# Performance work log

Measured on AMD Instinct MI355X. Metric: run time of the kernel, lower is better.

The kernel has to match this reference:

```python
import jax, jax.numpy as jnp
import numpy as np

HEADS = 8
REL_MAX = 64  # module-level constant REL_MAX_DIST


def _to_c(x):
    # x: [..., 2] real/imag interleaved (torch.view_as_real layout) -> complex
    return jax.lax.complex(x[..., 0], x[..., 1])


def setup_inputs() -> dict:
    key = jax.random.key(0)
    ks = jax.random.split(key, 12)
    dim, past_len = 256, 65536
    d2 = dim * 2
    s = 1.0 / np.sqrt(d2)  # torch Linear default init range

    def lin(k):
        kw, kb = jax.random.split(k)
        W = jax.random.uniform(kw, (d2, d2), jnp.float32, -s, s)
        b = jax.random.uniform(kb, (d2,), jnp.float32, -s, s)
        return W, b

    Wq, bq = lin(ks[0])
    Wk, bk = lin(ks[1])
    Wv, bv = lin(ks[2])
    Wo, bo = lin(ks[3])
    return {
        "curr_pos": past_len,
        "z_curr": jax.random.normal(ks[4], (dim, 2), jnp.float32),
        "z_past": jax.random.normal(ks[5], (past_len, dim, 2), jnp.float32),
        "Wq": Wq, "bq": bq, "Wk": Wk, "bk": bk,
        "Wv": Wv, "bv": bv, "Wo": Wo, "bo": bo,
        "rel_bias": jax.random.normal(ks[6], (2 * REL_MAX + 1, dim, 2), jnp.float32) * 0.02,
    }


def reference(curr_pos, z_curr, z_past, Wq, bq, Wk, bk, Wv, bv, Wo, bo, rel_bias):
    dim = z_curr.shape[0]
    past_len = z_past.shape[0]
    head_dim = dim // HEADS

    # real-valued linear projections on interleaved (real, imag) features
    q_proj = z_curr.reshape(-1) @ Wq.T + bq                        # [2*dim]
    k_proj = z_past.reshape(past_len, -1) @ Wk.T + bk              # [L, 2*dim]
    v_proj = z_past.reshape(past_len, -1) @ Wv.T + bv              # [L, 2*dim]

    # view as complex, split heads
    q_h = _to_c(q_proj.reshape(dim, 2)).reshape(HEADS, head_dim)               # [H, hd]
    k_h = _to_c(k_proj.reshape(past_len, dim, 2)).reshape(past_len, HEADS, head_dim)
    v_h = _to_c(v_proj.reshape(past_len, dim, 2)).reshape(past_len, HEADS, head_dim)

    # Re(<q, k>) per head
    dot_scores = jnp.real(jnp.conj(q_h)[None] * k_h).sum(-1)       # [L, H]

    # relative positional bias (gather + clamp)
    rel_dists = jnp.arange(curr_pos - past_len, curr_pos)
    idx = jnp.clip(rel_dists + REL_MAX, 0, 2 * REL_MAX)
    rb_h = _to_c(rel_bias)[idx].reshape(past_len, HEADS, head_dim)
    rel_scores = jnp.real(jnp.conj(q_h)[None] * rb_h).sum(-1)      # [L, H]

    scores = (dot_scores + rel_scores) / np.sqrt(head_dim)
    weights = jax.nn.softmax(scores, axis=0)                       # softmax over past_len

    out_h = (weights[..., None] * v_h).sum(0)                      # [H, hd] complex
    out_c = out_h.reshape(dim)
    out_real = jnp.stack([jnp.real(out_c), jnp.imag(out_c)], -1).reshape(-1)  # [2*dim]
    out = out_real @ Wo.T + bo
    # return real view [dim, 2] of the complex output (view_as_complex layout)
    return out.reshape(dim, 2)
```

## Files before the change

### kernel.cpp

```cpp
#include <hip/hip_runtime.h>
#include <math.h>


static constexpr float SCALE = 0.17677669529663687f;

__device__ __forceinline__ float wave_sum(float v) {
#pragma unroll
  for (int off = 32; off > 0; off >>= 1) v += __shfl_xor(v, off, 64);
  return v;
}

__global__ __launch_bounds__(256) void k_matvec512(
    const float* __restrict__ M, const float* __restrict__ x,
    const float* __restrict__ bias, float* __restrict__ y) {
  const int wave = threadIdx.x >> 6, lane = threadIdx.x & 63;
  const int j = blockIdx.x * 4 + wave;
  const float* Mr = M + (size_t)j * 512 + lane * 8;
  const float4 m0 = *(const float4*)Mr;
  const float4 m1 = *(const float4*)(Mr + 4);
  const float4 x0 = *(const float4*)(x + lane * 8);
  const float4 x1 = *(const float4*)(x + lane * 8 + 4);
  float acc = m0.x * x0.x + m0.y * x0.y + m0.z * x0.z + m0.w * x0.w +
              m1.x * x1.x + m1.y * x1.y + m1.z * x1.z + m1.w * x1.w;
  acc = wave_sum(acc);
  if (lane == 0) y[j] = acc + bias[j];
}

__global__ __launch_bounds__(256) void k_wkpart(
    const float* __restrict__ Wk, const float* __restrict__ qp,
    float* __restrict__ wkpart) {
  __shared__ float ql[32];
  const int b = blockIdx.x;
  if (threadIdx.x < 32) ql[threadIdx.x] = qp[b * 32 + threadIdx.x];
  __syncthreads();
  for (int i = threadIdx.x; i < 512; i += 256) {
    float acc = 0.f;
#pragma unroll
    for (int k = 0; k < 32; ++k)
      acc += ql[k] * Wk[(size_t)(b * 32 + k) * 512 + i];
    wkpart[b * 512 + i] = acc;
  }
}

__global__ __launch_bounds__(256) void k_misc(
    const float* __restrict__ qp, const float* __restrict__ bk,
    const float* __restrict__ rb, const float* __restrict__ wkpart,
    float* __restrict__ wk, float* __restrict__ ck, float* __restrict__ relq,
    float* __restrict__ S_un) {
  const int b = blockIdx.x;
  if (b < 8) {
    for (int i = threadIdx.x; i < 512; i += 256)
      wk[b * 512 + i] =
          (wkpart[(2 * b) * 512 + i] + wkpart[(2 * b + 1) * 512 + i]) * SCALE;
  } else if (b == 8) {
    if (threadIdx.x < 8) {
      const int h = threadIdx.x;
      float acc = 0.f;
      for (int k = 0; k < 64; ++k) acc += qp[h * 64 + k] * bk[h * 64 + k];
      ck[h] = acc * SCALE;
    }
  } else if (b < 14) {
    const int t = (b - 9) * 256 + threadIdx.x;
    if (t < 129 * 8) {
      const int idx = t >> 3, h = t & 7;
      float acc = 0.f;
      for (int k = 0; k < 64; ++k)
        acc += qp[h * 64 + k] * rb[(size_t)idx * 512 + h * 64 + k];
      relq[t] = acc * SCALE;
    }
  } else {
    for (int t = threadIdx.x; t < 4096; t += 256) S_un[t] = 0.f;
  }
}

__global__ __launch_bounds__(256, 2) void k_attn(
    const float* __restrict__ zp, const float* __restrict__ wk,
    const float* __restrict__ ck, const float* __restrict__ relq,
    const int* __restrict__ curr_pos, int L, float* __restrict__ Sp,
    float* __restrict__ sp) {
  __shared__ float relql[1032];
  __shared__ float Sl[4096];
  __shared__ float sl[4][8];
  const int tid = threadIdx.x;
  const int wave = tid >> 6, lane = tid & 63;
  for (int t = tid; t < 1032; t += 256) relql[t] = relq[t];

  float wkr[8][8];
#pragma unroll
  for (int h = 0; h < 8; ++h) {
    const float4 a = *(const float4*)(wk + h * 512 + lane * 8);
    const float4 b = *(const float4*)(wk + h * 512 + lane * 8 + 4);
    wkr[h][0] = a.x; wkr[h][1] = a.y; wkr[h][2] = a.z; wkr[h][3] = a.w;
    wkr[h][4] = b.x; wkr[h][5] = b.y; wkr[h][6] = b.z; wkr[h][7] = b.w;
  }
  const int myh = ((lane & 1) << 2) | (lane & 2) | ((lane >> 2) & 1);
  const float ck_my = ck[myh];
  const int cp = curr_pos[0];
  __syncthreads();

  float S[8][8];
#pragma unroll
  for (int h = 0; h < 8; ++h)
#pragma unroll
    for (int k = 0; k < 8; ++k) S[h][k] = 0.f;
  float s_loc = 0.f;

  const int l0 = blockIdx.x * 128 + wave * 32;
  const float* zr = zp + (size_t)l0 * 512 + lane * 8;
  float4 p0 = *(const float4*)zr;
  float4 p1 = *(const float4*)(zr + 4);

#pragma unroll 2
  for (int r = 0; r < 32; ++r) {
    const int l = l0 + r;
    const float* zn = (l + 1 < L) ? (zr + 512) : zr;
    const float4 n0 = *(const float4*)zn;
    const float4 n1 = *(const float4*)(zn + 4);
    const float zz[8] = {p0.x, p0.y, p0.z, p0.w, p1.x, p1.y, p1.z, p1.w};
    float acc[8];
#pragma unroll
    for (int h = 0; h < 8; ++h) {
      float a = 0.f;
#pragma unroll
      for (int k = 0; k < 8; ++k) a += zz[k] * wkr[h][k];
      acc[h] = a;
    }
    const bool lo1 = (lane & 1) == 0;
    float b0 = (lo1 ? acc[0] : acc[4]) + __shfl_xor(lo1 ? acc[4] : acc[0], 1, 64);
    float b1 = (lo1 ? acc[1] : acc[5]) + __shfl_xor(lo1 ? acc[5] : acc[1], 1, 64);
    float b2 = (lo1 ? acc[2] : acc[6]) + __shfl_xor(lo1 ? acc[6] : acc[2], 1, 64);
    float b3 = (lo1 ? acc[3] : acc[7]) + __shfl_xor(lo1 ? acc[7] : acc[3], 1, 64);
    const bool lo2 = (lane & 2) == 0;
    float c0 = (lo2 ? b0 : b2) + __shfl_xor(lo2 ? b2 : b0, 2, 64);
    float c1 = (lo2 ? b1 : b3) + __shfl_xor(lo2 ? b3 : b1, 2, 64);
    const bool lo3 = (lane & 4) == 0;
    float d = (lo3 ? c0 : c1) + __shfl_xor(lo3 ? c1 : c0, 4, 64);
    d += __shfl_xor(d, 8, 64);
    d += __shfl_xor(d, 16, 64);
    d += __shfl_xor(d, 32, 64);

    int dd = cp - L + l + 64;
    dd = dd < 0 ? 0 : (dd > 128 ? 128 : dd);
    float w = __expf(d + ck_my + relql[dd * 8 + myh]);
    if (l >= L) w = 0.f;
    s_loc += w;
#pragma unroll
    for (int h = 0; h < 8; ++h) {
      const int src = ((h & 1) << 2) | (h & 2) | ((h >> 2) & 1);
      const float wh = __shfl(w, src, 64);
#pragma unroll
      for (int k = 0; k < 8; ++k) S[h][k] += wh * zz[k];
    }
    p0 = n0; p1 = n1; zr += 512;
  }

  if (lane < 8) sl[wave][myh] = s_loc;
  for (int wv = 0; wv < 4; ++wv) {
    if (wave == wv) {
#pragma unroll
      for (int h = 0; h < 8; ++h)
#pragma unroll
        for (int k = 0; k < 8; ++k) {
          const int idx = h * 512 + lane * 8 + k;
          if (wv == 0) Sl[idx] = S[h][k];
          else Sl[idx] += S[h][k];
        }
    }
    __syncthreads();
  }
  for (int t = tid; t < 4096; t += 256)
    Sp[(size_t)blockIdx.x * 4096 + t] = Sl[t];
  if (tid < 8)
    sp[blockIdx.x * 8 + tid] = sl[0][tid] + sl[1][tid] + sl[2][tid] + sl[3][tid];
}

__global__ __launch_bounds__(256) void k_comb2(
    const float* __restrict__ Sp, const float* __restrict__ spv, int nb,
    float* __restrict__ S_un, float* __restrict__ s) {
  if (blockIdx.x < 256) {
    const int T = blockIdx.x * 256 + threadIdx.x;
    const int col = T & 4095;
    const int g = T >> 12;
    const int chunk = (nb + 15) >> 4;
    const int r0 = g * chunk;
    const int r1 = min(r0 + chunk, nb);
    float a[8];
#pragma unroll
    for (int u = 0; u < 8; ++u) a[u] = 0.f;
    int b = r0;
    for (; b + 8 <= r1; b += 8) {
#pragma unroll
      for (int u = 0; u < 8; ++u) a[u] += Sp[(size_t)(b + u) * 4096 + col];
    }
    for (; b < r1; ++b) a[0] += Sp[(size_t)b * 4096 + col];
    const float t = ((a[0] + a[1]) + (a[2] + a[3])) +
                    ((a[4] + a[5]) + (a[6] + a[7]));
    atomicAdd(&S_un[col], t);
  } else {
    __shared__ float red[256];
    float a = 0.f;
    for (int b2 = threadIdx.x >> 3; b2 < nb; b2 += 32)
      a += spv[b2 * 8 + (threadIdx.x & 7)];
    red[threadIdx.x] = a;
    __syncthreads();
    if (threadIdx.x < 8) {
      float x = 0.f;
      for (int c = 0; c < 32; ++c) x += red[c * 8 + threadIdx.x];
      s[threadIdx.x] = x;
    }
  }
}

__global__ __launch_bounds__(256) void k_outreal(
    const float* __restrict__ Wv, const float* __restrict__ S_un,
    const float* __restrict__ s, const float* __restrict__ bv,
    float* __restrict__ out_real) {
  const int wave = threadIdx.x >> 6, lane = threadIdx.x & 63;
  const int j = blockIdx.x * 4 + wave;
  const int h = j >> 6;
  const float* Mr = Wv + (size_t)j * 512 + lane * 8;
  const float* xr = S_un + h * 512 + lane * 8;
  const float4 m0 = *(const float4*)Mr;
  const float4 m1 = *(const float4*)(Mr + 4);
  const float4 x0 = *(const float4*)xr;
  const float4 x1 = *(const float4*)(xr + 4);
  float acc = m0.x * x0.x + m0.y * x0.y + m0.z * x0.z + m0.w * x0.w +
              m1.x * x1.x + m1.y * x1.y + m1.z * x1.z + m1.w * x1.w;
  acc = wave_sum(acc);
  if (lane == 0) out_real[j] = acc / s[h] + bv[j];
}

extern "C" void kernel_launch(void* const* d_in, const int* in_sizes, int n_in,
                              void* d_out, int out_size, void* d_ws,
                              size_t ws_size, hipStream_t stream) {
  const int* curr_pos = (const int*)d_in[0];
  const float* z_curr = (const float*)d_in[1];
  const float* z_past = (const float*)d_in[2];
  const float* Wq = (const float*)d_in[3];
  const float* bq = (const float*)d_in[4];
  const float* Wk = (const float*)d_in[5];
  const float* bk = (const float*)d_in[6];
  const float* Wv = (const float*)d_in[7];
  const float* bv = (const float*)d_in[8];
  const float* Wo = (const float*)d_in[9];
  const float* bo = (const float*)d_in[10];
  const float* rb = (const float*)d_in[11];
  float* out = (float*)d_out;

  const int L = in_sizes[2] / 512;
  const int nb = (L + 127) / 128;

  float* ws = (float*)d_ws;
  size_t o = 0;
  float* qp = ws + o;       o += 512;
  float* wkpart = ws + o;   o += 16 * 512;
  float* wk = ws + o;       o += 8 * 512;
  float* ck = ws + o;       o += 16;
  float* relq = ws + o;     o += 1040;
  float* s = ws + o;        o += 8;
  float* sp = ws + o;       o += (size_t)nb * 8;
  float* S_un = ws + o;     o += 4096;
  float* out_real = ws + o; o += 512;
  float* Sp = ws + o;       o += (size_t)nb * 4096;
  (void)ws_size; (void)n_in; (void)out_size;

  k_matvec512<<<128, 256, 0, stream>>>(Wq, z_curr, bq, qp);
  k_wkpart<<<16, 256, 0, stream>>>(Wk, qp, wkpart);
  k_misc<<<15, 256, 0, stream>>>(qp, bk, rb, wkpart, wk, ck, relq, S_un);
  k_attn<<<nb, 256, 0, stream>>>(z_past, wk, ck, relq, curr_pos, L, Sp, sp);
  k_comb2<<<257, 256, 0, stream>>>(Sp, sp, nb, S_un, s);
  k_outreal<<<128, 256, 0, stream>>>(Wv, S_un, s, bv, out_real);
  k_matvec512<<<128, 256, 0, stream>>>(Wo, out_real, bo, out);
}
```

Baseline: 243.4 us.

## Fuse front kernels, atomically reduce attention partials, prefetch two rows ahead

The change merges the Wk-projection partial and misc setup kernels into one launch, with each block reducing a full head so the separate partial-sum pass goes away. The attention kernel now adds its per-block sums straight into the global accumulator with atomics, which removes the Sp scratch write and the k_comb2 reduction kernel. The z_past prefetch is also deepened to two rows ahead. The cost is heavy atomic contention, since 512 blocks each add into the same 4096 floats, plus nondeterministic summation order and extra registers for the deeper prefetch.

```diff
diff --git a/kernel.cpp b/kernel.cpp
--- a/kernel.cpp
+++ b/kernel.cpp
@@ -26,58 +26,53 @@
   if (lane == 0) y[j] = acc + bias[j];
 }
 
-__global__ __launch_bounds__(256) void k_wkpart(
+__global__ __launch_bounds__(256) void k_front2(
     const float* __restrict__ Wk, const float* __restrict__ qp,
-    float* __restrict__ wkpart) {
-  __shared__ float ql[32];
+    const float* __restrict__ bk, const float* __restrict__ rb,
+    float* __restrict__ wk, float* __restrict__ ck, float* __restrict__ relq,
+    float* __restrict__ S_un, float* __restrict__ s) {
+  __shared__ float ql[512];
   const int b = blockIdx.x;
-  if (threadIdx.x < 32) ql[threadIdx.x] = qp[b * 32 + threadIdx.x];
-  __syncthreads();
-  for (int i = threadIdx.x; i < 512; i += 256) {
+  if (b < 16) {
+    const int h = b >> 1;
+    if (threadIdx.x < 64) ql[threadIdx.x] = qp[h * 64 + threadIdx.x];
+    __syncthreads();
+    const int i = (b & 1) * 256 + threadIdx.x;
     float acc = 0.f;
 #pragma unroll
-    for (int k = 0; k < 32; ++k)
-      acc += ql[k] * Wk[(size_t)(b * 32 + k) * 512 + i];
-    wkpart[b * 512 + i] = acc;
-  }
-}
-
-__global__ __launch_bounds__(256) void k_misc(
-    const float* __restrict__ qp, const float* __restrict__ bk,
-    const float* __restrict__ rb, const float* __restrict__ wkpart,
-    float* __restrict__ wk, float* __restrict__ ck, float* __restrict__ relq,
-    float* __restrict__ S_un) {
-  const int b = blockIdx.x;
-  if (b < 8) {
-    for (int i = threadIdx.x; i < 512; i += 256)
-      wk[b * 512 + i] =
-          (wkpart[(2 * b) * 512 + i] + wkpart[(2 * b + 1) * 512 + i]) * SCALE;
-  } else if (b == 8) {
+    for (int k = 0; k < 64; ++k)
+      acc += ql[k] * Wk[(size_t)(h * 64 + k) * 512 + i];
+    wk[h * 512 + i] = acc * SCALE;
+  } else if (b < 22) {
+    for (int t = threadIdx.x; t < 512; t += 256) ql[t] = qp[t];
+    __syncthreads();
+    const int t = (b - 16) * 256 + threadIdx.x;
+    if (t < 129 * 8) {
+      const int idx = t >> 3, h = t & 7;
+      float acc = 0.f;
+#pragma unroll
+      for (int k = 0; k < 64; ++k)
+        acc += ql[h * 64 + k] * rb[(size_t)idx * 512 + h * 64 + k];
+      relq[t] = acc * SCALE;
+    }
+  } else if (b == 22) {
     if (threadIdx.x < 8) {
       const int h = threadIdx.x;
       float acc = 0.f;
       for (int k = 0; k < 64; ++k) acc += qp[h * 64 + k] * bk[h * 64 + k];
       ck[h] = acc * SCALE;
     }
-  } else if (b < 14) {
-    const int t = (b - 9) * 256 + threadIdx.x;
-    if (t < 129 * 8) {
-      const int idx = t >> 3, h = t & 7;
-      float acc = 0.f;
-      for (int k = 0; k < 64; ++k)
-        acc += qp[h * 64 + k] * rb[(size_t)idx * 512 + h * 64 + k];
-      relq[t] = acc * SCALE;
-    }
   } else {
     for (int t = threadIdx.x; t < 4096; t += 256) S_un[t] = 0.f;
+    if (threadIdx.x < 8) s[threadIdx.x] = 0.f;
   }
 }
 
 __global__ __launch_bounds__(256, 2) void k_attn(
     const float* __restrict__ zp, const float* __restrict__ wk,
     const float* __restrict__ ck, const float* __restrict__ relq,
-    const int* __restrict__ curr_pos, int L, float* __restrict__ Sp,
-    float* __restrict__ sp) {
+    const int* __restrict__ curr_pos, int L, float* __restrict__ S_un,
+    float* __restrict__ s_out) {
   __shared__ float relql[1032];
   __shared__ float Sl[4096];
   __shared__ float sl[4][8];
@@ -109,11 +104,14 @@
   const float* zr = zp + (size_t)l0 * 512 + lane * 8;
   float4 p0 = *(const float4*)zr;
   float4 p1 = *(const float4*)(zr + 4);
+  const float* z1p = (l0 + 1 < L) ? (zr + 512) : zr;
+  float4 q0 = *(const float4*)z1p;
+  float4 q1 = *(const float4*)(z1p + 4);
 
 #pragma unroll 2
   for (int r = 0; r < 32; ++r) {
     const int l = l0 + r;
-    const float* zn = (l + 1 < L) ? (zr + 512) : zr;
+    const float* zn = (l + 2 < L) ? (zr + 1024) : zr;
     const float4 n0 = *(const float4*)zn;
     const float4 n1 = *(const float4*)(zn + 4);
     const float zz[8] = {p0.x, p0.y, p0.z, p0.w, p1.x, p1.y, p1.z, p1.w};
@@ -151,7 +149,7 @@
 #pragma unroll
       for (int k = 0; k < 8; ++k) S[h][k] += wh * zz[k];
     }
-    p0 = n0; p1 = n1; zr += 512;
+    p0 = q0; p1 = q1; q0 = n0; q1 = n1; zr += 512;
   }
 
   if (lane < 8) sl[wave][myh] = s_loc;
@@ -168,47 +166,9 @@
     }
     __syncthreads();
   }
-  for (int t = tid; t < 4096; t += 256)
-    Sp[(size_t)blockIdx.x * 4096 + t] = Sl[t];
+  for (int t = tid; t < 4096; t += 256) atomicAdd(&S_un[t], Sl[t]);
   if (tid < 8)
-    sp[blockIdx.x * 8 + tid] = sl[0][tid] + sl[1][tid] + sl[2][tid] + sl[3][tid];
-}
-
-__global__ __launch_bounds__(256) void k_comb2(
-    const float* __restrict__ Sp, const float* __restrict__ spv, int nb,
-    float* __restrict__ S_un, float* __restrict__ s) {
-  if (blockIdx.x < 256) {
-    const int T = blockIdx.x * 256 + threadIdx.x;
-    const int col = T & 4095;
-    const int g = T >> 12;
-    const int chunk = (nb + 15) >> 4;
-    const int r0 = g * chunk;
-    const int r1 = min(r0 + chunk, nb);
-    float a[8];
-#pragma unroll
-    for (int u = 0; u < 8; ++u) a[u] = 0.f;
-    int b = r0;
-    for (; b + 8 <= r1; b += 8) {
-#pragma unroll
-      for (int u = 0; u < 8; ++u) a[u] += Sp[(size_t)(b + u) * 4096 + col];
-    }
-    for (; b < r1; ++b) a[0] += Sp[(size_t)b * 4096 + col];
-    const float t = ((a[0] + a[1]) + (a[2] + a[3])) +
-                    ((a[4] + a[5]) + (a[6] + a[7]));
-    atomicAdd(&S_un[col], t);
-  } else {
-    __shared__ float red[256];
-    float a = 0.f;
-    for (int b2 = threadIdx.x >> 3; b2 < nb; b2 += 32)
-      a += spv[b2 * 8 + (threadIdx.x & 7)];
-    red[threadIdx.x] = a;
-    __syncthreads();
-    if (threadIdx.x < 8) {
-      float x = 0.f;
-      for (int c = 0; c < 32; ++c) x += red[c * 8 + threadIdx.x];
-      s[threadIdx.x] = x;
-    }
-  }
+    atomicAdd(&s_out[tid], sl[0][tid] + sl[1][tid] + sl[2][tid] + sl[3][tid]);
 }
 
 __global__ __launch_bounds__(256) void k_outreal(
@@ -253,22 +213,17 @@
   float* ws = (float*)d_ws;
   size_t o = 0;
   float* qp = ws + o;       o += 512;
-  float* wkpart = ws + o;   o += 16 * 512;
-  float* wk = ws + o;       o += 8 * 512;
-  float* ck = ws + o;       o += 16;
+  float* wkb = ws + o;      o += 8 * 512;
+  float* ckb = ws + o;      o += 16;
   float* relq = ws + o;     o += 1040;
-  float* s = ws + o;        o += 8;
-  float* sp = ws + o;       o += (size_t)nb * 8;
+  float* sb = ws + o;       o += 8;
   float* S_un = ws + o;     o += 4096;
   float* out_real = ws + o; o += 512;
-  float* Sp = ws + o;       o += (size_t)nb * 4096;
   (void)ws_size; (void)n_in; (void)out_size;
 
   k_matvec512<<<128, 256, 0, stream>>>(Wq, z_curr, bq, qp);
-  k_wkpart<<<16, 256, 0, stream>>>(Wk, qp, wkpart);
-  k_misc<<<15, 256, 0, stream>>>(qp, bk, rb, wkpart, wk, ck, relq, S_un);
-  k_attn<<<nb, 256, 0, stream>>>(z_past, wk, ck, relq, curr_pos, L, Sp, sp);
-  k_comb2<<<257, 256, 0, stream>>>(Sp, sp, nb, S_un, s);
-  k_outreal<<<128, 256, 0, stream>>>(Wv, S_un, s, bv, out_real);
+  k_front2<<<24, 256, 0, stream>>>(Wk, qp, bk, rb, wkb, ckb, relq, S_un, sb);
+  k_attn<<<nb, 256, 0, stream>>>(z_past, wkb, ckb, relq, curr_pos, L, S_un, sb);
+  k_outreal<<<128, 256, 0, stream>>>(Wv, S_un, sb, bv, out_real);
   k_matvec512<<<128, 256, 0, stream>>>(Wo, out_real, bo, out);
 }
```

Measured after the change: 260.4 us. 1.07x slower.
